# Performance work log

Measured on AMD Instinct MI355X. Metric: run time of the kernel, lower is better.

## Reference

```python
import jax, jax.numpy as jnp
import numpy as np

B, N = 256, 512
DIM_GRAPH = 256
DIM_DESC = 256
RANK = 64


def setup_inputs() -> dict:
    key = jax.random.key(0)
    ks = jax.random.split(key, 6)
    tokns_k = jax.random.normal(ks[0], (B, DIM_DESC), dtype=jnp.float32)
    H_pad = jax.random.normal(ks[1], (B, N, DIM_GRAPH), dtype=jnp.float32)
    mask = jax.random.randint(ks[2], (B, N), 0, 2).astype(bool)
    mask = mask.at[:, 0].set(True)  # ensure at least one valid node per graph
    # Linear weights, torch convention: y = x @ W.T
    Wq = jax.random.normal(ks[3], (RANK, DIM_DESC), dtype=jnp.float32) / np.sqrt(DIM_DESC)
    Wk = jax.random.normal(ks[4], (RANK, DIM_GRAPH), dtype=jnp.float32) / np.sqrt(DIM_GRAPH)
    Wv = jax.random.normal(ks[5], (DIM_DESC, DIM_GRAPH), dtype=jnp.float32) / np.sqrt(DIM_GRAPH)
    log_scale = jnp.zeros((1,), dtype=jnp.float32)
    return {"tokns_k": tokns_k, "H_pad": H_pad, "mask": mask,
            "Wq": Wq, "Wk": Wk, "Wv": Wv, "log_scale": log_scale}


def reference(tokns_k, H_pad, mask, Wq, Wk, Wv, log_scale):
    q = tokns_k @ Wq.T                                  # [B, r]
    k = jnp.einsum('bnd,rd->bnr', H_pad, Wk)            # [B, N, r]
    scale = jnp.maximum(jnp.exp(log_scale), 0.1)        # clamp(min=0.1)
    scores = jnp.einsum('br,bnr->bn', q, k) / scale     # [B, N]
    neg_inf = jnp.float32(-jnp.inf)
    scores = jnp.where(mask, scores, neg_inf)
    alpha = jax.nn.softmax(scores, axis=-1)             # [B, N]
    v = jnp.einsum('bnd,ed->bne', H_pad, Wv)            # [B, N, dim_desc]
    ctx_k = jnp.einsum('bn,bne->be', alpha, v)          # [B, dim_desc]
    return (alpha, ctx_k)
```

## Files before the change

kernel.cpp:

```cpp
#include <hip/hip_runtime.h>

constexpr int Bc = 256;
constexpr int Nc = 512;
constexpr int Dc = 256;
constexpr int Rc = 64;
constexpr int SPLIT = 8;
constexpr int ROWS = Nc / SPLIT;
constexpr int GROUP = 32;

constexpr size_t WS_P = 0;
constexpr size_t WS_L = WS_P + (size_t)Bc * Dc;
constexpr size_t WS_H = WS_L + (size_t)Bc * SPLIT;
constexpr size_t WS_FLOATS = WS_H + (size_t)Bc * SPLIT * Dc;

__global__ __launch_bounds__(256) void k0_precompute_p(
    const float* __restrict__ tokns_k, const float* __restrict__ Wq,
    const float* __restrict__ Wk, float* __restrict__ ws)
{
    const int b = blockIdx.x;
    const int t = threadIdx.x;
    const int wave = t >> 6, lane = t & 63, g = lane >> 4, l16 = lane & 15;

    __shared__ float q_s[Rc];

    #pragma unroll
    for (int step = 0; step < 4; ++step) {
        const int r = wave * 16 + step * 4 + g;
        float acc = 0.0f;
        #pragma unroll
        for (int j = 0; j < 4; ++j) {
            const float4 tk = *(const float4*)(tokns_k + b * Dc + l16 * 4 + j * 64);
            const float4 wq = *(const float4*)(Wq + r * Dc + l16 * 4 + j * 64);
            acc += tk.x * wq.x + tk.y * wq.y + tk.z * wq.z + tk.w * wq.w;
        }
        #pragma unroll
        for (int off = 1; off < 16; off <<= 1) acc += __shfl_xor(acc, off);
        if (l16 == 0) q_s[r] = acc;
    }
    __syncthreads();

    float acc = 0.0f;
    #pragma unroll 8
    for (int r = 0; r < Rc; ++r) acc += q_s[r] * Wk[r * Dc + t];
    ws[WS_P + (size_t)b * Dc + t] = acc;
}

__global__ __launch_bounds__(256) void k1_stream(
    const float* __restrict__ H_pad, const int* __restrict__ mask,
    const float* __restrict__ log_scale, float* __restrict__ ws,
    float* __restrict__ out)
{
    const int s = blockIdx.x;
    const int b = blockIdx.y;
    const int t = threadIdx.x;
    const int n0 = s * ROWS;

    const int rowA = t >> 3;
    const int e    = t & 7;
    const int tau  = t >> 4;
    const int l16  = t & 15;

    __shared__ __align__(16) float hm[16][Dc];
    __shared__ float pn_s[ROWS];
    __shared__ float scores_s[ROWS];
    __shared__ int   mask_s[ROWS];

    if (t < ROWS) mask_s[t] = mask[b * Nc + n0 + t];

    const float inv_scale = 1.0f / fmaxf(__expf(log_scale[0]), 0.1f);

    const float* __restrict__ pb = ws + WS_P + (size_t)b * Dc;
    float4 pA[8];
    #pragma unroll
    for (int k = 0; k < 8; ++k) pA[k] = *(const float4*)(pb + (e + 8 * k) * 4);

    const float* __restrict__ Hb = H_pad + ((size_t)b * Nc + n0) * Dc;

    float4 h4[4];
    #pragma unroll
    for (int j = 0; j < 4; ++j) h4[j] = make_float4(0.f, 0.f, 0.f, 0.f);

    __syncthreads();

    #pragma unroll
    for (int g = 0; g < ROWS / GROUP; ++g) {
        {
            const int n = g * GROUP + rowA;
            const float* __restrict__ row = Hb + n * Dc;
            float4 x[8];
            #pragma unroll
            for (int k = 0; k < 8; ++k) x[k] = *(const float4*)(row + (e + 8 * k) * 4);
            float acc = 0.0f;
            #pragma unroll
            for (int k = 0; k < 8; ++k)
                acc += x[k].x * pA[k].x + x[k].y * pA[k].y
                     + x[k].z * pA[k].z + x[k].w * pA[k].w;
            acc += __shfl_xor(acc, 1);
            acc += __shfl_xor(acc, 2);
            acc += __shfl_xor(acc, 4);
            acc *= inv_scale;
            if (mask_s[n] == 0) acc = -1e30f;
            if (e == 0) {
                scores_s[n] = acc;
                pn_s[n] = __expf(acc);
            }
        }
        __syncthreads();

        #pragma unroll
        for (int r = 0; r < 2; ++r) {
            const int n = g * GROUP + tau * 2 + r;
            const float pn = pn_s[n];
            const float* __restrict__ row = Hb + n * Dc;
            #pragma unroll
            for (int j = 0; j < 4; ++j) {
                const float4 x = *(const float4*)(row + (l16 + 16 * j) * 4);
                h4[j].x = fmaf(pn, x.x, h4[j].x);
                h4[j].y = fmaf(pn, x.y, h4[j].y);
                h4[j].z = fmaf(pn, x.z, h4[j].z);
                h4[j].w = fmaf(pn, x.w, h4[j].w);
            }
        }
    }

    #pragma unroll
    for (int j = 0; j < 4; ++j) *(float4*)(&hm[tau][(l16 + 16 * j) * 4]) = h4[j];
    __syncthreads();

    if (t < ROWS) out[b * Nc + n0 + t] = scores_s[t];
    if (t < ROWS) {
        float L = pn_s[t];
        #pragma unroll
        for (int off = 32; off >= 1; off >>= 1) L += __shfl_xor(L, off);
        if (t == 0) ws[WS_L + (size_t)b * SPLIT + s] = L;
    }
    float hsum = 0.0f;
    #pragma unroll
    for (int p = 0; p < 16; ++p) hsum += hm[p][t];
    ws[WS_H + ((size_t)b * SPLIT + s) * Dc + t] = hsum;
}

__global__ __launch_bounds__(256) void k2_merge(
    const float* __restrict__ Wv, const float* __restrict__ ws,
    float* __restrict__ out)
{
    const int b = blockIdx.x;
    const int t = threadIdx.x;
    const int wave = t >> 6, lane = t & 63, g = lane >> 4, l16 = lane & 15;

    __shared__ __align__(16) float hbar[Dc];

    float L = 0.0f;
    #pragma unroll
    for (int s = 0; s < SPLIT; ++s) L += ws[WS_L + (size_t)b * SPLIT + s];
    const float invL = 1.0f / L;

    float hacc = 0.0f;
    #pragma unroll
    for (int s = 0; s < SPLIT; ++s) hacc += ws[WS_H + ((size_t)b * SPLIT + s) * Dc + t];
    hbar[t] = hacc * invL;

    #pragma unroll
    for (int i = 0; i < Nc / 256; ++i) {
        const int idx = b * Nc + i * 256 + t;
        out[idx] = __expf(out[idx]) * invL;
    }
    __syncthreads();

    float4 hb4[4];
    #pragma unroll
    for (int j = 0; j < 4; ++j) hb4[j] = *(const float4*)(hbar + l16 * 4 + j * 64);
    float* __restrict__ ctx_out = out + (size_t)Bc * Nc + b * Dc;
    #pragma unroll
    for (int step = 0; step < 16; ++step) {
        const int e = step * 16 + wave * 4 + g;
        float acc = 0.0f;
        #pragma unroll
        for (int j = 0; j < 4; ++j) {
            const float4 wv = *(const float4*)(Wv + e * Dc + l16 * 4 + j * 64);
            acc += wv.x * hb4[j].x + wv.y * hb4[j].y + wv.z * hb4[j].z + wv.w * hb4[j].w;
        }
        #pragma unroll
        for (int off = 1; off < 16; off <<= 1) acc += __shfl_xor(acc, off);
        if (l16 == 0) ctx_out[e] = acc;
    }
}

constexpr int FNT = 512;
constexpr int FNW = FNT / 64;
constexpr int FNPW = Nc / FNW;

__global__ __launch_bounds__(FNT) void fba_fallback(
    const float* __restrict__ tokns_k, const float* __restrict__ H_pad,
    const int* __restrict__ mask, const float* __restrict__ Wq,
    const float* __restrict__ Wk, const float* __restrict__ Wv,
    const float* __restrict__ log_scale, float* __restrict__ out)
{
    const int b = blockIdx.x, t = threadIdx.x;
    const int wave = t >> 6, lane = t & 63;

    __shared__ __align__(16) float q_s[Rc];
    __shared__ __align__(16) float p_s[Dc];
    __shared__ __align__(16) float scores_s[Nc];
    __shared__ __align__(16) float hmerge[FNW][Dc];
    __shared__ float l_s[FNW];
    __shared__ __align__(16) float hbar[Dc];
    __shared__ int mask_s[Nc];

    const float inv_scale = 1.0f / fmaxf(__expf(log_scale[0]), 0.1f);

    const float4 tok4 = *(const float4*)(tokns_k + b * Dc + lane * 4);
    #pragma unroll
    for (int i = 0; i < Rc / FNW; ++i) {
        const int r = wave * (Rc / FNW) + i;
        const float4 w4 = *(const float4*)(Wq + r * Dc + lane * 4);
        float s = w4.x * tok4.x + w4.y * tok4.y + w4.z * tok4.z + w4.w * tok4.w;
        #pragma unroll
        for (int off = 32; off >= 1; off >>= 1) s += __shfl_xor(s, off);
        if (lane == 0) q_s[r] = s;
    }
    mask_s[t] = mask[b * Nc + t];
    mask_s[t + FNT] = mask[b * Nc + t + FNT];
    __syncthreads();

    if (t < Dc) {
        float acc = 0.0f;
        #pragma unroll 8
        for (int r = 0; r < Rc; ++r) acc += q_s[r] * Wk[r * Dc + t];
        p_s[t] = acc;
    }
    __syncthreads();

    const float4 p4 = *(const float4*)(p_s + lane * 4);
    const float* Hb = H_pad + (size_t)b * Nc * Dc;
    float l_acc = 0.0f;
    float4 h4 = make_float4(0.f, 0.f, 0.f, 0.f);

    for (int i = 0; i < FNPW; ++i) {
        const int n = wave * FNPW + i;
        const float4 x4 = *(const float4*)(Hb + n * Dc + lane * 4);
        float s = x4.x * p4.x + x4.y * p4.y + x4.z * p4.z + x4.w * p4.w;
        #pragma unroll
        for (int off = 32; off >= 1; off >>= 1) s += __shfl_xor(s, off);
        s *= inv_scale;
        if (mask_s[n] == 0) s = -1e30f;
        if (lane == 0) scores_s[n] = s;
        const float pn = __expf(s);
        l_acc += pn;
        h4.x = fmaf(pn, x4.x, h4.x); h4.y = fmaf(pn, x4.y, h4.y);
        h4.z = fmaf(pn, x4.z, h4.z); h4.w = fmaf(pn, x4.w, h4.w);
    }

    if (lane == 0) l_s[wave] = l_acc;
    *(float4*)(&hmerge[wave][lane * 4]) = h4;
    __syncthreads();

    float L = 0.0f;
    #pragma unroll
    for (int w = 0; w < FNW; ++w) L += l_s[w];
    const float invL = 1.0f / L;

    if (t < Dc) {
        float acc = 0.0f;
        #pragma unroll
        for (int w = 0; w < FNW; ++w) acc += hmerge[w][t];
        hbar[t] = acc * invL;
    }
    out[b * Nc + t] = __expf(scores_s[t]) * invL;
    out[b * Nc + t + FNT] = __expf(scores_s[t + FNT]) * invL;
    __syncthreads();

    const float4 hb4 = *(const float4*)(hbar + lane * 4);
    float* ctx_out = out + (size_t)Bc * Nc + b * Dc;
    #pragma unroll
    for (int i = 0; i < Dc / FNW; ++i) {
        const int e = wave * (Dc / FNW) + i;
        const float4 w4 = *(const float4*)(Wv + e * Dc + lane * 4);
        float s = w4.x * hb4.x + w4.y * hb4.y + w4.z * hb4.z + w4.w * hb4.w;
        #pragma unroll
        for (int off = 32; off >= 1; off >>= 1) s += __shfl_xor(s, off);
        if (lane == 0) ctx_out[e] = s;
    }
}

extern "C" void kernel_launch(void* const* d_in, const int* in_sizes, int n_in,
                              void* d_out, int out_size, void* d_ws, size_t ws_size,
                              hipStream_t stream) {
    const float* tokns_k   = (const float*)d_in[0];
    const float* H_pad     = (const float*)d_in[1];
    const int*   mask      = (const int*)d_in[2];
    const float* Wq        = (const float*)d_in[3];
    const float* Wk        = (const float*)d_in[4];
    const float* Wv        = (const float*)d_in[5];
    const float* log_scale = (const float*)d_in[6];
    float* out = (float*)d_out;

    if (ws_size >= WS_FLOATS * sizeof(float)) {
        float* ws = (float*)d_ws;
        k0_precompute_p<<<Bc, 256, 0, stream>>>(tokns_k, Wq, Wk, ws);
        dim3 grid1(SPLIT, Bc);
        k1_stream<<<grid1, 256, 0, stream>>>(H_pad, mask, log_scale, ws, out);
        k2_merge<<<Bc, 256, 0, stream>>>(Wv, ws, out);
    } else {
        fba_fallback<<<Bc, FNT, 0, stream>>>(tokns_k, H_pad, mask, Wq, Wk, Wv,
                                             log_scale, out);
    }
}
```

Measured before the change: 227.5 us.

## Restructure stream kernel so each wave owns 16 rows for scores and accumulation

The stream kernel is reorganised so each wave computes scores for its own 16 rows, using 4 lanes per row and a projection vector staged in shared memory. It then accumulates the weighted H rows with one float4 per lane across the full feature width. This removes the group loop with its per-group barriers, cuts the partial-sum buffer from 16 to 4 slices, and lowers register pressure from the held projection registers. The trade-off is that every row of H is now read twice from global memory in separate phases, relying on cache hits, and the projection vector is re-read from shared memory on every iteration.

```diff
diff --git a/kernel.cpp b/kernel.cpp
--- a/kernel.cpp
+++ b/kernel.cpp
@@ -6,7 +6,6 @@
 constexpr int Rc = 64;
 constexpr int SPLIT = 8;
 constexpr int ROWS = Nc / SPLIT;
-constexpr int GROUP = 32;
 
 constexpr size_t WS_P = 0;
 constexpr size_t WS_L = WS_P + (size_t)Bc * Dc;
@@ -53,78 +52,60 @@
     const int s = blockIdx.x;
     const int b = blockIdx.y;
     const int t = threadIdx.x;
+    const int wave = t >> 6, lane = t & 63;
+    const int l4   = lane & 3;
+    const int roww = lane >> 2;
     const int n0 = s * ROWS;
 
-    const int rowA = t >> 3;
-    const int e    = t & 7;
-    const int tau  = t >> 4;
-    const int l16  = t & 15;
-
-    __shared__ __align__(16) float hm[16][Dc];
+    __shared__ __align__(16) float p_s[Dc];
+    __shared__ __align__(16) float hm[4][Dc];
     __shared__ float pn_s[ROWS];
     __shared__ float scores_s[ROWS];
     __shared__ int   mask_s[ROWS];
 
+    p_s[t] = ws[WS_P + (size_t)b * Dc + t];
     if (t < ROWS) mask_s[t] = mask[b * Nc + n0 + t];
-
     const float inv_scale = 1.0f / fmaxf(__expf(log_scale[0]), 0.1f);
-
-    const float* __restrict__ pb = ws + WS_P + (size_t)b * Dc;
-    float4 pA[8];
-    #pragma unroll
-    for (int k = 0; k < 8; ++k) pA[k] = *(const float4*)(pb + (e + 8 * k) * 4);
+    __syncthreads();
 
     const float* __restrict__ Hb = H_pad + ((size_t)b * Nc + n0) * Dc;
 
-    float4 h4[4];
-    #pragma unroll
-    for (int j = 0; j < 4; ++j) h4[j] = make_float4(0.f, 0.f, 0.f, 0.f);
-
-    __syncthreads();
-
-    #pragma unroll
-    for (int g = 0; g < ROWS / GROUP; ++g) {
-        {
-            const int n = g * GROUP + rowA;
-            const float* __restrict__ row = Hb + n * Dc;
-            float4 x[8];
-            #pragma unroll
-            for (int k = 0; k < 8; ++k) x[k] = *(const float4*)(row + (e + 8 * k) * 4);
-            float acc = 0.0f;
-            #pragma unroll
-            for (int k = 0; k < 8; ++k)
-                acc += x[k].x * pA[k].x + x[k].y * pA[k].y
-                     + x[k].z * pA[k].z + x[k].w * pA[k].w;
-            acc += __shfl_xor(acc, 1);
-            acc += __shfl_xor(acc, 2);
-            acc += __shfl_xor(acc, 4);
-            acc *= inv_scale;
-            if (mask_s[n] == 0) acc = -1e30f;
-            if (e == 0) {
-                scores_s[n] = acc;
-                pn_s[n] = __expf(acc);
-            }
-        }
-        __syncthreads();
-
-        #pragma unroll
-        for (int r = 0; r < 2; ++r) {
-            const int n = g * GROUP + tau * 2 + r;
-            const float pn = pn_s[n];
-            const float* __restrict__ row = Hb + n * Dc;
-            #pragma unroll
-            for (int j = 0; j < 4; ++j) {
-                const float4 x = *(const float4*)(row + (l16 + 16 * j) * 4);
-                h4[j].x = fmaf(pn, x.x, h4[j].x);
-                h4[j].y = fmaf(pn, x.y, h4[j].y);
-                h4[j].z = fmaf(pn, x.z, h4[j].z);
-                h4[j].w = fmaf(pn, x.w, h4[j].w);
-            }
-        }
-    }
-
-    #pragma unroll
-    for (int j = 0; j < 4; ++j) *(float4*)(&hm[tau][(l16 + 16 * j) * 4]) = h4[j];
+    {
+        const int row = wave * 16 + roww;
+        const float* __restrict__ rptr = Hb + row * Dc;
+        float acc = 0.0f;
+        #pragma unroll
+        for (int j = 0; j < 16; ++j) {
+            const int c = l4 + 4 * j;
+            const float4 x  = *(const float4*)(rptr + c * 4);
+            const float4 pp = *(const float4*)(p_s + c * 4);
+            acc += x.x * pp.x + x.y * pp.y + x.z * pp.z + x.w * pp.w;
+        }
+        acc += __shfl_xor(acc, 1);
+        acc += __shfl_xor(acc, 2);
+        acc *= inv_scale;
+        if (mask_s[row] == 0) acc = -1e30f;
+        if (l4 == 0) {
+            scores_s[row] = acc;
+            pn_s[row] = __expf(acc);
+        }
+    }
+    __syncthreads();
+
+    {
+        float4 h4 = make_float4(0.f, 0.f, 0.f, 0.f);
+        #pragma unroll
+        for (int r = 0; r < 16; ++r) {
+            const int row = wave * 16 + r;
+            const float pn = pn_s[row];
+            const float4 x = *(const float4*)(Hb + row * Dc + lane * 4);
+            h4.x = fmaf(pn, x.x, h4.x);
+            h4.y = fmaf(pn, x.y, h4.y);
+            h4.z = fmaf(pn, x.z, h4.z);
+            h4.w = fmaf(pn, x.w, h4.w);
+        }
+        *(float4*)(&hm[wave][lane * 4]) = h4;
+    }
     __syncthreads();
 
     if (t < ROWS) out[b * Nc + n0 + t] = scores_s[t];
@@ -134,10 +115,8 @@
         for (int off = 32; off >= 1; off >>= 1) L += __shfl_xor(L, off);
         if (t == 0) ws[WS_L + (size_t)b * SPLIT + s] = L;
     }
-    float hsum = 0.0f;
-    #pragma unroll
-    for (int p = 0; p < 16; ++p) hsum += hm[p][t];
-    ws[WS_H + ((size_t)b * SPLIT + s) * Dc + t] = hsum;
+    ws[WS_H + ((size_t)b * SPLIT + s) * Dc + t] =
+        (hm[0][t] + hm[1][t]) + (hm[2][t] + hm[3][t]);
 }
 
 __global__ __launch_bounds__(256) void k2_merge(
```

Result: no change. 227.6 us (+0.0%).
